# Optimization experiments

Measured on AMD Instinct MI355X. Metric: run time of the kernel, lower is better.

The kernel has to match this reference:

```python
import jax, jax.numpy as jnp
import numpy as np

N_NODES = 50000
N_EDGES = 800000
IN_DIM = 128
HID_DIM = 128
N_CLASSES = 40


def setup_inputs() -> dict:
    key = jax.random.key(0)
    ks = jax.random.split(key, 12)
    s = 0.05
    inp = {
        "X": jax.random.normal(ks[0], (N_NODES, IN_DIM), jnp.float32),
        "A": jax.random.randint(ks[1], (2, N_EDGES), 0, N_NODES, dtype=jnp.int64),
        "W0": jax.random.normal(ks[2], (HID_DIM, IN_DIM), jnp.float32) * s,
        "b0": jnp.zeros((HID_DIM,), jnp.float32),
        "W1": jax.random.normal(ks[3], (HID_DIM, HID_DIM), jnp.float32) * s,
        "b1": jnp.zeros((HID_DIM,), jnp.float32),
        "W2": jax.random.normal(ks[4], (HID_DIM, HID_DIM), jnp.float32) * s,
        "b2": jnp.zeros((HID_DIM,), jnp.float32),
        "W3": jax.random.normal(ks[5], (HID_DIM, HID_DIM), jnp.float32) * s,
        "b3": jnp.zeros((HID_DIM,), jnp.float32),
        "Wf": jax.random.normal(ks[6], (N_CLASSES, HID_DIM), jnp.float32) * s,
        "bf": jnp.zeros((N_CLASSES,), jnp.float32),
    }
    return inp


def _gcn_conv(x, W, b, src, dst):
    # FrobeniusNormGCNConv: normalize weight by Frobenius norm, then standard GCNConv
    Wn = W / jnp.linalg.norm(W)
    h = x @ Wn.T  # [N, out]
    # gcn_norm with self-loops (edge weight 1.0): deg over targets + 1 self loop
    ones = jnp.ones((dst.shape[0],), h.dtype)
    deg = jax.ops.segment_sum(ones, dst, num_segments=N_NODES) + 1.0
    dinv = jax.lax.rsqrt(deg)  # [N]
    norm = dinv[src] * dinv[dst]  # [E]
    # scatter-add of normalized source messages into targets
    agg = jax.ops.segment_sum(norm[:, None] * h[src], dst, num_segments=N_NODES)
    # self-loop contribution: dinv[i]^2 * h[i]; bias added after aggregation
    return agg + (dinv * dinv)[:, None] * h + b


def reference(X, A, W0, b0, W1, b1, W2, b2, W3, b3, Wf, bf):
    src, dst = A[0], A[1]
    h = _gcn_conv(X, W0, b0, src, dst)
    skip = h
    for W, b in ((W1, b1), (W2, b2), (W3, b3)):
        h = _gcn_conv(h, W, b, src, dst)
        h = jax.nn.relu(h)
        h = h + skip  # residual skip (dropout identity in eval mode)
        skip = h
    return h @ Wf.T + bf
```

## Files before the change

kernel.cpp:

```cpp
#include <hip/hip_runtime.h>

#define N_NODES_C 50000
#define N_EDGES_C 800000
#define DIM 128
#define NCLS 40
#define SCAN_NB ((N_NODES_C + 255) / 256)
#define NBUK 32
#define BCAP 32768

typedef __attribute__((ext_vector_type(8))) short bf16x8;
typedef __attribute__((ext_vector_type(4))) float f32x4;

__device__ inline float bf2f(unsigned short u) {
    union { unsigned int i; float f; } c;
    c.i = ((unsigned int)u) << 16;
    return c.f;
}
__device__ inline unsigned short f2bf(float f) {
    union { float f; unsigned int i; } c;
    c.f = f;
    unsigned int x = c.i;
    x += 0x7fffu + ((x >> 16) & 1u);
    return (unsigned short)(x >> 16);
}
__device__ inline void unp8(const uint4& g, float* f) {
    f[0] = __uint_as_float(g.x << 16); f[1] = __uint_as_float(g.x & 0xFFFF0000u);
    f[2] = __uint_as_float(g.y << 16); f[3] = __uint_as_float(g.y & 0xFFFF0000u);
    f[4] = __uint_as_float(g.z << 16); f[5] = __uint_as_float(g.z & 0xFFFF0000u);
    f[6] = __uint_as_float(g.w << 16); f[7] = __uint_as_float(g.w & 0xFFFF0000u);
}

__global__ __launch_bounds__(256) void k_pre(const float* __restrict__ W0,
                                             const float* __restrict__ W1,
                                             const float* __restrict__ W2,
                                             const float* __restrict__ W3,
                                             unsigned short* __restrict__ Wb,
                                             float* __restrict__ scale_inv,
                                             int* __restrict__ gcount) {
    int b = blockIdx.x;
    if (b < 64) {
        int m = b >> 4;
        int idx = (b & 15) * 256 + threadIdx.x;
        const float* W = m == 0 ? W0 : m == 1 ? W1 : m == 2 ? W2 : W3;
        float4 v = reinterpret_cast<const float4*>(W)[idx];
        reinterpret_cast<ushort4*>(Wb + (size_t)m * DIM * DIM)[idx] =
            make_ushort4(f2bf(v.x), f2bf(v.y), f2bf(v.z), f2bf(v.w));
        return;
    }
    b -= 64;
    if (b == 0 && threadIdx.x < NBUK) gcount[threadIdx.x] = 0;
    const float* W = b == 0 ? W0 : b == 1 ? W1 : b == 2 ? W2 : W3;
    float s = 0.f;
    for (int i = threadIdx.x; i < DIM * DIM; i += 256) {
        float v = W[i];
        s += v * v;
    }
    #pragma unroll
    for (int off = 32; off >= 1; off >>= 1) s += __shfl_down(s, off);
    __shared__ float red[4];
    int lane = threadIdx.x & 63, wid = threadIdx.x >> 6;
    if (lane == 0) red[wid] = s;
    __syncthreads();
    if (threadIdx.x == 0) {
        float tot = red[0] + red[1] + red[2] + red[3];
        scale_inv[b] = 1.0f / sqrtf(tot);
    }
}

__global__ __launch_bounds__(256) void k_bucket(const int* __restrict__ A,
                                                int* __restrict__ gcount,
                                                unsigned int* __restrict__ ebuk, int E) {
    __shared__ int cnt[NBUK];
    __shared__ int gbase[NBUK];
    int tid = threadIdx.x;
    if (tid < NBUK) cnt[tid] = 0;
    __syncthreads();
    int e0 = blockIdx.x * 1024;
    int s[4], d[4], b[4], r[4];
    #pragma unroll
    for (int j = 0; j < 4; ++j) {
        int e = e0 + j * 256 + tid;
        if (e < E) {
            s[j] = A[e];
            d[j] = A[E + e];
            b[j] = (int)(((unsigned long long)(unsigned)d[j] * NBUK) / N_NODES_C);
            r[j] = atomicAdd(&cnt[b[j]], 1);
        } else {
            b[j] = -1;
        }
    }
    __syncthreads();
    if (tid < NBUK) gbase[tid] = atomicAdd(&gcount[tid], cnt[tid]);
    __syncthreads();
    #pragma unroll
    for (int j = 0; j < 4; ++j) {
        if (b[j] >= 0) {
            int pos = gbase[b[j]] + r[j];
            if (pos < BCAP)
                ebuk[(size_t)b[j] * BCAP + pos] =
                    ((unsigned)d[j] << 16) | (unsigned)s[j];
        }
    }
}

__global__ __launch_bounds__(256) void k_degb(const unsigned int* __restrict__ ebuk,
                                              const int* __restrict__ gcount,
                                              int* __restrict__ deg) {
    int k = blockIdx.x;
    int base = (k * N_NODES_C + NBUK - 1) / NBUK;
    int next = ((k + 1) * N_NODES_C + NBUK - 1) / NBUK;
    int sz = next - base;
    __shared__ int dl[1568];
    for (int i = threadIdx.x; i < sz; i += 256) dl[i] = 0;
    __syncthreads();
    int count = gcount[k];
    if (count > BCAP) count = BCAP;
    for (int i = threadIdx.x; i < count; i += 256) {
        int d = (int)(ebuk[(size_t)k * BCAP + i] >> 16);
        atomicAdd(&dl[d - base], 1);
    }
    __syncthreads();
    for (int i = threadIdx.x; i < sz; i += 256) deg[base + i] = dl[i];
}

__global__ __launch_bounds__(256) void k_scan_part(const int* __restrict__ cnt,
                                                   int* __restrict__ partial,
                                                   float* __restrict__ dinv,
                                                   int* __restrict__ fill, int n) {
    int idx = blockIdx.x * 256 + threadIdx.x;
    int v = (idx < n) ? cnt[idx] : 0;
    if (idx < n) {
        dinv[idx] = rsqrtf((float)v + 1.0f);
        fill[idx] = 0;
    }
    int s = v;
    #pragma unroll
    for (int off = 32; off >= 1; off >>= 1) s += __shfl_down(s, off);
    __shared__ int red[4];
    int lane = threadIdx.x & 63, wid = threadIdx.x >> 6;
    if (lane == 0) red[wid] = s;
    __syncthreads();
    if (threadIdx.x == 0) partial[blockIdx.x] = red[0] + red[1] + red[2] + red[3];
}

__global__ __launch_bounds__(256) void k_scan_final(const int* __restrict__ cnt,
                                                    const int* __restrict__ partial,
                                                    int* __restrict__ ptr, int n, int nb) {
    int tid = threadIdx.x, bid = blockIdx.x;
    int lane = tid & 63, wid = tid >> 6;
    int pv = (tid < nb) ? partial[tid] : 0;
    int vb = (tid < bid) ? pv : 0;
    int s1 = vb, s2 = pv;
    #pragma unroll
    for (int off = 32; off >= 1; off >>= 1) {
        s1 += __shfl_down(s1, off);
        s2 += __shfl_down(s2, off);
    }
    __shared__ int r1[4], r2[4];
    if (lane == 0) { r1[wid] = s1; r2[wid] = s2; }
    __syncthreads();
    __shared__ int sbase, stot;
    if (tid == 0) {
        sbase = r1[0] + r1[1] + r1[2] + r1[3];
        stot  = r2[0] + r2[1] + r2[2] + r2[3];
    }
    __syncthreads();
    int idx = bid * 256 + tid;
    int v = (idx < n) ? cnt[idx] : 0;
    int sc = v;
    #pragma unroll
    for (int off = 1; off < 64; off <<= 1) {
        int t = __shfl_up(sc, off);
        if (lane >= off) sc += t;
    }
    __shared__ int wsum[4], wpre[4];
    if (lane == 63) wsum[wid] = sc;
    __syncthreads();
    if (tid == 0) {
        int acc = 0;
        #pragma unroll
        for (int w = 0; w < 4; ++w) { wpre[w] = acc; acc += wsum[w]; }
    }
    __syncthreads();
    if (idx < n) ptr[idx] = sbase + wpre[wid] + sc - v;
    if (bid == 0 && tid == 0) ptr[n] = stot;
}

__global__ __launch_bounds__(256) void k_fillb(const unsigned int* __restrict__ ebuk,
                                               const int* __restrict__ gcount,
                                               const int* __restrict__ ptr,
                                               int* __restrict__ fill,
                                               unsigned short* __restrict__ esrc) {
    int k = blockIdx.x & (NBUK - 1);
    int c = blockIdx.x / NBUK;
    int count = gcount[k];
    if (count > BCAP) count = BCAP;
    int i0 = c * 1024;
    if (i0 >= count) return;
    #pragma unroll
    for (int j = 0; j < 4; ++j) {
        int i = i0 + j * 256 + threadIdx.x;
        if (i < count) {
            unsigned v = ebuk[(size_t)k * BCAP + i];
            int d = (int)(v >> 16);
            int s = (int)(v & 0xFFFFu);
            int pos = ptr[d] + atomicAdd(&fill[d], 1);
            esrc[pos] = (unsigned short)s;
        }
    }
}

template <bool F32A>
__global__ __launch_bounds__(256) void k_gemm_mfma(const void* __restrict__ Xp,
                                                   const unsigned short* __restrict__ Wb,
                                                   const float* __restrict__ scale_ptr,
                                                   const float* __restrict__ dinv,
                                                   unsigned short* __restrict__ Gb, int N) {
    int tid = threadIdx.x;
    int w = tid >> 6;
    int l = tid & 63;
    int l15 = l & 15;
    int lg = l >> 4;
    int arow = blockIdx.x * 64 + w * 16 + l15;
    if (arow >= N) arow = N - 1;
    float scale = scale_ptr[0];

    f32x4 acc[8];
    #pragma unroll
    for (int ct = 0; ct < 8; ++ct) acc[ct] = f32x4{0.f, 0.f, 0.f, 0.f};

    #pragma unroll
    for (int kc = 0; kc < 4; ++kc) {
        int ko = kc * 32 + lg * 8;
        bf16x8 a;
        if (F32A) {
            const float4* xf = reinterpret_cast<const float4*>(
                (const float*)Xp + (size_t)arow * DIM + ko);
            float4 u = xf[0], v = xf[1];
            a[0] = (short)f2bf(u.x); a[1] = (short)f2bf(u.y);
            a[2] = (short)f2bf(u.z); a[3] = (short)f2bf(u.w);
            a[4] = (short)f2bf(v.x); a[5] = (short)f2bf(v.y);
            a[6] = (short)f2bf(v.z); a[7] = (short)f2bf(v.w);
        } else {
            a = *reinterpret_cast<const bf16x8*>(
                (const unsigned short*)Xp + (size_t)arow * DIM + ko);
        }
        #pragma unroll
        for (int ct = 0; ct < 8; ++ct) {
            bf16x8 b = *reinterpret_cast<const bf16x8*>(&Wb[(size_t)(ct * 16 + l15) * DIM + ko]);
            acc[ct] = __builtin_amdgcn_mfma_f32_16x16x32_bf16(a, b, acc[ct], 0, 0, 0);
        }
    }
    int outrow0 = blockIdx.x * 64 + w * 16 + lg * 4;
    #pragma unroll
    for (int r = 0; r < 4; ++r) {
        int row = outrow0 + r;
        if (row < N) {
            float dv = dinv[row] * scale;
            #pragma unroll
            for (int ct = 0; ct < 8; ++ct)
                Gb[(size_t)row * DIM + ct * 16 + l15] = f2bf(acc[ct][r] * dv);
        }
    }
}

template <bool RELU>
__global__ __launch_bounds__(256) void k_agg(const unsigned short* __restrict__ Gb,
                                             const float* __restrict__ bias,
                                             const float* __restrict__ dinv,
                                             const int* __restrict__ ptr,
                                             const unsigned short* __restrict__ esrc,
                                             const unsigned short* __restrict__ skipb,
                                             unsigned short* __restrict__ outb) {
    int n = blockIdx.x * 4 + (threadIdx.x >> 6);
    int l = threadIdx.x & 63;
    int grp = l >> 4, li = l & 15;
    const uint4* __restrict__ Gv = reinterpret_cast<const uint4*>(Gb);
    int beg = ptr[n], end = ptr[n + 1];
    float acc[8] = {};
    float t[8];
    int e = beg;
    for (; e + 16 <= end; e += 16) {
        int s0 = esrc[e + grp];
        int s1 = esrc[e + 4 + grp];
        int s2 = esrc[e + 8 + grp];
        int s3 = esrc[e + 12 + grp];
        uint4 g0 = Gv[(size_t)s0 * 16 + li];
        uint4 g1 = Gv[(size_t)s1 * 16 + li];
        uint4 g2 = Gv[(size_t)s2 * 16 + li];
        uint4 g3 = Gv[(size_t)s3 * 16 + li];
        unp8(g0, t);
        #pragma unroll
        for (int j = 0; j < 8; ++j) acc[j] += t[j];
        unp8(g1, t);
        #pragma unroll
        for (int j = 0; j < 8; ++j) acc[j] += t[j];
        unp8(g2, t);
        #pragma unroll
        for (int j = 0; j < 8; ++j) acc[j] += t[j];
        unp8(g3, t);
        #pragma unroll
        for (int j = 0; j < 8; ++j) acc[j] += t[j];
    }
    for (; e + 4 <= end; e += 4) {
        int s0 = esrc[e + grp];
        uint4 g0 = Gv[(size_t)s0 * 16 + li];
        unp8(g0, t);
        #pragma unroll
        for (int j = 0; j < 8; ++j) acc[j] += t[j];
    }
    int rem = end - e;
    if (grp < rem) {
        int s0 = esrc[e + grp];
        uint4 g0 = Gv[(size_t)s0 * 16 + li];
        unp8(g0, t);
        #pragma unroll
        for (int j = 0; j < 8; ++j) acc[j] += t[j];
    }
    #pragma unroll
    for (int j = 0; j < 8; ++j) {
        acc[j] += __shfl_xor(acc[j], 16);
        acc[j] += __shfl_xor(acc[j], 32);
    }
    if (grp == 0) {
        float di = dinv[n];
        uint4 gu = Gv[(size_t)n * 16 + li];
        float gs[8];
        unp8(gu, gs);
        const float4* b4 = reinterpret_cast<const float4*>(bias);
        float4 ba = b4[li * 2], bb = b4[li * 2 + 1];
        float bv[8] = {ba.x, ba.y, ba.z, ba.w, bb.x, bb.y, bb.z, bb.w};
        float v[8];
        #pragma unroll
        for (int j = 0; j < 8; ++j) v[j] = fmaf(di, acc[j] + gs[j], bv[j]);
        if (RELU) {
            uint4 su = reinterpret_cast<const uint4*>(skipb)[(size_t)n * 16 + li];
            float ss[8];
            unp8(su, ss);
            #pragma unroll
            for (int j = 0; j < 8; ++j) v[j] = fmaxf(v[j], 0.f) + ss[j];
        }
        uint4 o;
        o.x = (unsigned)f2bf(v[0]) | ((unsigned)f2bf(v[1]) << 16);
        o.y = (unsigned)f2bf(v[2]) | ((unsigned)f2bf(v[3]) << 16);
        o.z = (unsigned)f2bf(v[4]) | ((unsigned)f2bf(v[5]) << 16);
        o.w = (unsigned)f2bf(v[6]) | ((unsigned)f2bf(v[7]) << 16);
        reinterpret_cast<uint4*>(outb)[(size_t)n * 16 + li] = o;
    }
}

__global__ __launch_bounds__(256) void k_final(const unsigned short* __restrict__ Hb,
                                               const float* __restrict__ Wf,
                                               const float* __restrict__ bf,
                                               float* __restrict__ out, int N) {
    __shared__ float Xs[16][68];
    __shared__ float Ws[16][64];
    int tid = threadIdx.x;
    int n0 = blockIdx.x * 64;
    int tx = tid & 15;
    int ty = tid >> 4;
    float acc[4][4] = {};
    for (int k0 = 0; k0 < DIM; k0 += 16) {
        {
            int j = tid >> 2, kq = tid & 3;
            int row = n0 + j;
            if (row >= N) row = N - 1;
            ushort4 x4 = *reinterpret_cast<const ushort4*>(&Hb[(size_t)row * DIM + k0 + kq * 4]);
            Xs[kq * 4 + 0][j] = bf2f(x4.x);
            Xs[kq * 4 + 1][j] = bf2f(x4.y);
            Xs[kq * 4 + 2][j] = bf2f(x4.z);
            Xs[kq * 4 + 3][j] = bf2f(x4.w);
        }
        {
            int o = tid >> 2, kq = tid & 3;
            int om = o < NCLS ? o : o - NCLS;
            const float4 w4 = *reinterpret_cast<const float4*>(&Wf[(size_t)om * DIM + k0 + kq * 4]);
            Ws[kq * 4 + 0][o] = w4.x;
            Ws[kq * 4 + 1][o] = w4.y;
            Ws[kq * 4 + 2][o] = w4.z;
            Ws[kq * 4 + 3][o] = w4.w;
        }
        __syncthreads();
        #pragma unroll
        for (int k = 0; k < 16; ++k) {
            float4 w = *reinterpret_cast<const float4*>(&Ws[k][tx * 4]);
            float4 x = *reinterpret_cast<const float4*>(&Xs[k][ty * 4]);
            float xv[4] = {x.x, x.y, x.z, x.w};
            #pragma unroll
            for (int i = 0; i < 4; ++i) {
                acc[i][0] = fmaf(xv[i], w.x, acc[i][0]);
                acc[i][1] = fmaf(xv[i], w.y, acc[i][1]);
                acc[i][2] = fmaf(xv[i], w.z, acc[i][2]);
                acc[i][3] = fmaf(xv[i], w.w, acc[i][3]);
            }
        }
        __syncthreads();
    }
    if (tx >= 10) return;
    float4 b4 = make_float4(bf[tx * 4], bf[tx * 4 + 1], bf[tx * 4 + 2], bf[tx * 4 + 3]);
    #pragma unroll
    for (int i = 0; i < 4; ++i) {
        int row = n0 + ty * 4 + i;
        if (row < N) {
            float* op = &out[(size_t)row * NCLS + tx * 4];
            op[0] = acc[i][0] + b4.x;
            op[1] = acc[i][1] + b4.y;
            op[2] = acc[i][2] + b4.z;
            op[3] = acc[i][3] + b4.w;
        }
    }
}

extern "C" void kernel_launch(void* const* d_in, const int* in_sizes, int n_in,
                              void* d_out, int out_size, void* d_ws, size_t ws_size,
                              hipStream_t stream) {
    (void)in_sizes; (void)n_in; (void)out_size; (void)ws_size;
    const float* X  = (const float*)d_in[0];
    const int*   A  = (const int*)d_in[1];
    const float* W0 = (const float*)d_in[2];
    const float* b0 = (const float*)d_in[3];
    const float* W1 = (const float*)d_in[4];
    const float* b1 = (const float*)d_in[5];
    const float* W2 = (const float*)d_in[6];
    const float* b2 = (const float*)d_in[7];
    const float* W3 = (const float*)d_in[8];
    const float* b3 = (const float*)d_in[9];
    const float* Wf = (const float*)d_in[10];
    const float* bf = (const float*)d_in[11];
    float* out = (float*)d_out;

    char* base_ws = (char*)d_ws;
    size_t off = 0;
    auto alloc = [&](size_t bytes) -> char* {
        char* p = base_ws + off;
        off = (off + bytes + 255) & ~(size_t)255;
        return p;
    };
    float* scale_inv = (float*)alloc(4 * sizeof(float));
    int*   deg    = (int*)alloc(N_NODES_C * sizeof(int));
    int*   fill   = (int*)alloc(N_NODES_C * sizeof(int));
    int*   ptr    = (int*)alloc((N_NODES_C + 1) * sizeof(int));
    float* dinv   = (float*)alloc(N_NODES_C * sizeof(float));
    int*   part   = (int*)alloc(SCAN_NB * sizeof(int));
    int*   gcount = (int*)alloc(NBUK * sizeof(int));
    unsigned int*   ebuk = (unsigned int*)alloc((size_t)NBUK * BCAP * sizeof(unsigned int));
    unsigned short* esrc = (unsigned short*)alloc((size_t)N_EDGES_C * sizeof(unsigned short));
    unsigned short* Gb  = (unsigned short*)alloc((size_t)N_NODES_C * DIM * sizeof(unsigned short));
    unsigned short* Hb1 = (unsigned short*)alloc((size_t)N_NODES_C * DIM * sizeof(unsigned short));
    unsigned short* Hb2 = (unsigned short*)alloc((size_t)N_NODES_C * DIM * sizeof(unsigned short));
    unsigned short* Wb  = (unsigned short*)alloc((size_t)4 * DIM * DIM * sizeof(unsigned short));

    k_pre<<<68, 256, 0, stream>>>(W0, W1, W2, W3, Wb, scale_inv, gcount);
    k_bucket<<<(N_EDGES_C + 1023) / 1024, 256, 0, stream>>>(A, gcount, ebuk, N_EDGES_C);
    k_degb<<<NBUK, 256, 0, stream>>>(ebuk, gcount, deg);
    k_scan_part<<<SCAN_NB, 256, 0, stream>>>(deg, part, dinv, fill, N_NODES_C);
    k_scan_final<<<SCAN_NB, 256, 0, stream>>>(deg, part, ptr, N_NODES_C, SCAN_NB);
    k_fillb<<<NBUK * (BCAP / 1024), 256, 0, stream>>>(ebuk, gcount, ptr, fill, esrc);

    const int gemm_grid = (N_NODES_C + 63) / 64;
    const int agg_grid  = N_NODES_C / 4;

    k_gemm_mfma<true><<<gemm_grid, 256, 0, stream>>>(X, Wb + 0 * DIM * DIM, scale_inv + 0, dinv, Gb, N_NODES_C);
    k_agg<false><<<agg_grid, 256, 0, stream>>>(Gb, b0, dinv, ptr, esrc, nullptr, Hb1);
    k_gemm_mfma<false><<<gemm_grid, 256, 0, stream>>>(Hb1, Wb + 1 * DIM * DIM, scale_inv + 1, dinv, Gb, N_NODES_C);
    k_agg<true><<<agg_grid, 256, 0, stream>>>(Gb, b1, dinv, ptr, esrc, Hb1, Hb2);
    k_gemm_mfma<false><<<gemm_grid, 256, 0, stream>>>(Hb2, Wb + 2 * DIM * DIM, scale_inv + 2, dinv, Gb, N_NODES_C);
    k_agg<true><<<agg_grid, 256, 0, stream>>>(Gb, b2, dinv, ptr, esrc, Hb2, Hb1);
    k_gemm_mfma<false><<<gemm_grid, 256, 0, stream>>>(Hb1, Wb + 3 * DIM * DIM, scale_inv + 3, dinv, Gb, N_NODES_C);
    k_agg<true><<<agg_grid, 256, 0, stream>>>(Gb, b3, dinv, ptr, esrc, Hb1, Hb2);
    k_final<<<(N_NODES_C + 63) / 64, 256, 0, stream>>>(Hb2, Wf, bf, out, N_NODES_C);
}
```

Baseline: 340.1 us.

## Fuse degree count, scan and CSR fill into one per-bucket kernel

Replaces the degree, two-pass scan and fill kernels with one kernel per destination bucket. Each block counts degrees in shared memory, split into octants by source index, scans them locally, and takes its global offset from bucket counts. It then places edges using shared-memory atomics, which also groups each node's sources by octant for better gather locality. This removes three launches and the global atomics and scratch arrays, but the CSR stage now runs on only 32 blocks.

After: 311.1 us. -8.5%, faster.

```diff
diff --git a/kernel.cpp b/kernel.cpp
--- a/kernel.cpp
+++ b/kernel.cpp
@@ -4,9 +4,9 @@
 #define N_EDGES_C 800000
 #define DIM 128
 #define NCLS 40
-#define SCAN_NB ((N_NODES_C + 255) / 256)
 #define NBUK 32
 #define BCAP 32768
+#define NOCT 8
 
 typedef __attribute__((ext_vector_type(8))) short bf16x8;
 typedef __attribute__((ext_vector_type(4))) float f32x4;
@@ -103,110 +103,94 @@
     }
 }
 
-__global__ __launch_bounds__(256) void k_degb(const unsigned int* __restrict__ ebuk,
-                                              const int* __restrict__ gcount,
-                                              int* __restrict__ deg) {
+__global__ __launch_bounds__(512) void k_csr(const unsigned int* __restrict__ ebuk,
+                                             const int* __restrict__ gcount,
+                                             int* __restrict__ ptr,
+                                             float* __restrict__ dinv,
+                                             unsigned short* __restrict__ esrc) {
+    __shared__ int dlo[NOCT][1568];
+    __shared__ int gc[NBUK];
+    __shared__ int wsum2[8], wpre2[8];
     int k = blockIdx.x;
+    int tid = threadIdx.x;
     int base = (k * N_NODES_C + NBUK - 1) / NBUK;
     int next = ((k + 1) * N_NODES_C + NBUK - 1) / NBUK;
     int sz = next - base;
-    __shared__ int dl[1568];
-    for (int i = threadIdx.x; i < sz; i += 256) dl[i] = 0;
-    __syncthreads();
-    int count = gcount[k];
-    if (count > BCAP) count = BCAP;
-    for (int i = threadIdx.x; i < count; i += 256) {
-        int d = (int)(ebuk[(size_t)k * BCAP + i] >> 16);
-        atomicAdd(&dl[d - base], 1);
-    }
-    __syncthreads();
-    for (int i = threadIdx.x; i < sz; i += 256) deg[base + i] = dl[i];
-}
-
-__global__ __launch_bounds__(256) void k_scan_part(const int* __restrict__ cnt,
-                                                   int* __restrict__ partial,
-                                                   float* __restrict__ dinv,
-                                                   int* __restrict__ fill, int n) {
-    int idx = blockIdx.x * 256 + threadIdx.x;
-    int v = (idx < n) ? cnt[idx] : 0;
-    if (idx < n) {
-        dinv[idx] = rsqrtf((float)v + 1.0f);
-        fill[idx] = 0;
-    }
-    int s = v;
-    #pragma unroll
-    for (int off = 32; off >= 1; off >>= 1) s += __shfl_down(s, off);
-    __shared__ int red[4];
-    int lane = threadIdx.x & 63, wid = threadIdx.x >> 6;
-    if (lane == 0) red[wid] = s;
-    __syncthreads();
-    if (threadIdx.x == 0) partial[blockIdx.x] = red[0] + red[1] + red[2] + red[3];
-}
-
-__global__ __launch_bounds__(256) void k_scan_final(const int* __restrict__ cnt,
-                                                    const int* __restrict__ partial,
-                                                    int* __restrict__ ptr, int n, int nb) {
-    int tid = threadIdx.x, bid = blockIdx.x;
+
+    for (int i = tid; i < NOCT * 1568; i += 512) (&dlo[0][0])[i] = 0;
+    if (tid < NBUK) gc[tid] = min(gcount[tid], BCAP);
+    __syncthreads();
+
+    int count = gc[k];
+    int bucket_base = 0;
+    #pragma unroll
+    for (int j = 0; j < NBUK; ++j) bucket_base += (j < k) ? gc[j] : 0;
+    const unsigned int* eb = ebuk + (size_t)k * BCAP;
+
+    for (int i = tid; i < count; i += 512) {
+        unsigned v = eb[i];
+        int d = (int)(v >> 16) - base;
+        int src = (int)(v & 0xFFFFu);
+        int oct = (src * NOCT) / N_NODES_C;
+        atomicAdd(&dlo[oct][d], 1);
+    }
+    __syncthreads();
+
+    int degloc[4];
+    int mysum = 0;
+    #pragma unroll
+    for (int c = 0; c < 4; ++c) {
+        int i = tid * 4 + c;
+        int ds = 0;
+        if (i < sz) {
+            #pragma unroll
+            for (int o = 0; o < NOCT; ++o) ds += dlo[o][i];
+        }
+        degloc[c] = ds;
+        mysum += ds;
+    }
     int lane = tid & 63, wid = tid >> 6;
-    int pv = (tid < nb) ? partial[tid] : 0;
-    int vb = (tid < bid) ? pv : 0;
-    int s1 = vb, s2 = pv;
-    #pragma unroll
-    for (int off = 32; off >= 1; off >>= 1) {
-        s1 += __shfl_down(s1, off);
-        s2 += __shfl_down(s2, off);
-    }
-    __shared__ int r1[4], r2[4];
-    if (lane == 0) { r1[wid] = s1; r2[wid] = s2; }
-    __syncthreads();
-    __shared__ int sbase, stot;
-    if (tid == 0) {
-        sbase = r1[0] + r1[1] + r1[2] + r1[3];
-        stot  = r2[0] + r2[1] + r2[2] + r2[3];
-    }
-    __syncthreads();
-    int idx = bid * 256 + tid;
-    int v = (idx < n) ? cnt[idx] : 0;
-    int sc = v;
+    int sc = mysum;
     #pragma unroll
     for (int off = 1; off < 64; off <<= 1) {
         int t = __shfl_up(sc, off);
         if (lane >= off) sc += t;
     }
-    __shared__ int wsum[4], wpre[4];
-    if (lane == 63) wsum[wid] = sc;
+    if (lane == 63) wsum2[wid] = sc;
     __syncthreads();
     if (tid == 0) {
-        int acc = 0;
-        #pragma unroll
-        for (int w = 0; w < 4; ++w) { wpre[w] = acc; acc += wsum[w]; }
-    }
-    __syncthreads();
-    if (idx < n) ptr[idx] = sbase + wpre[wid] + sc - v;
-    if (bid == 0 && tid == 0) ptr[n] = stot;
-}
-
-__global__ __launch_bounds__(256) void k_fillb(const unsigned int* __restrict__ ebuk,
-                                               const int* __restrict__ gcount,
-                                               const int* __restrict__ ptr,
-                                               int* __restrict__ fill,
-                                               unsigned short* __restrict__ esrc) {
-    int k = blockIdx.x & (NBUK - 1);
-    int c = blockIdx.x / NBUK;
-    int count = gcount[k];
-    if (count > BCAP) count = BCAP;
-    int i0 = c * 1024;
-    if (i0 >= count) return;
-    #pragma unroll
-    for (int j = 0; j < 4; ++j) {
-        int i = i0 + j * 256 + threadIdx.x;
-        if (i < count) {
-            unsigned v = ebuk[(size_t)k * BCAP + i];
-            int d = (int)(v >> 16);
-            int s = (int)(v & 0xFFFFu);
-            int pos = ptr[d] + atomicAdd(&fill[d], 1);
-            esrc[pos] = (unsigned short)s;
-        }
+        int a = 0;
+        #pragma unroll
+        for (int w = 0; w < 8; ++w) { wpre2[w] = a; a += wsum2[w]; }
+    }
+    __syncthreads();
+    int run = wpre2[wid] + sc - mysum;
+    #pragma unroll
+    for (int c = 0; c < 4; ++c) {
+        int i = tid * 4 + c;
+        if (i < sz) {
+            ptr[base + i] = bucket_base + run;
+            dinv[base + i] = rsqrtf((float)degloc[c] + 1.0f);
+            int r = run;
+            #pragma unroll
+            for (int o = 0; o < NOCT; ++o) {
+                int t = dlo[o][i];
+                dlo[o][i] = r;
+                r += t;
+            }
+            run += degloc[c];
+        }
+    }
+    if (k == NBUK - 1 && tid == 511) ptr[N_NODES_C] = bucket_base + run;
+    __syncthreads();
+
+    for (int i = tid; i < count; i += 512) {
+        unsigned v = eb[i];
+        int d = (int)(v >> 16) - base;
+        int src = (int)(v & 0xFFFFu);
+        int oct = (src * NOCT) / N_NODES_C;
+        int pos = atomicAdd(&dlo[oct][d], 1);
+        esrc[bucket_base + pos] = (unsigned short)src;
     }
 }
 
@@ -437,11 +421,8 @@
         return p;
     };
     float* scale_inv = (float*)alloc(4 * sizeof(float));
-    int*   deg    = (int*)alloc(N_NODES_C * sizeof(int));
-    int*   fill   = (int*)alloc(N_NODES_C * sizeof(int));
     int*   ptr    = (int*)alloc((N_NODES_C + 1) * sizeof(int));
     float* dinv   = (float*)alloc(N_NODES_C * sizeof(float));
-    int*   part   = (int*)alloc(SCAN_NB * sizeof(int));
     int*   gcount = (int*)alloc(NBUK * sizeof(int));
     unsigned int*   ebuk = (unsigned int*)alloc((size_t)NBUK * BCAP * sizeof(unsigned int));
     unsigned short* esrc = (unsigned short*)alloc((size_t)N_EDGES_C * sizeof(unsigned short));
@@ -452,10 +433,7 @@
 
     k_pre<<<68, 256, 0, stream>>>(W0, W1, W2, W3, Wb, scale_inv, gcount);
     k_bucket<<<(N_EDGES_C + 1023) / 1024, 256, 0, stream>>>(A, gcount, ebuk, N_EDGES_C);
-    k_degb<<<NBUK, 256, 0, stream>>>(ebuk, gcount, deg);
-    k_scan_part<<<SCAN_NB, 256, 0, stream>>>(deg, part, dinv, fill, N_NODES_C);
-    k_scan_final<<<SCAN_NB, 256, 0, stream>>>(deg, part, ptr, N_NODES_C, SCAN_NB);
-    k_fillb<<<NBUK * (BCAP / 1024), 256, 0, stream>>>(ebuk, gcount, ptr, fill, esrc);
+    k_csr<<<NBUK, 512, 0, stream>>>(ebuk, gcount, ptr, dinv, esrc);
 
     const int gemm_grid = (N_NODES_C + 63) / 64;
     const int agg_grid  = N_NODES_C / 4;
```
